# Kernel optimization log

Measured on AMD Instinct MI355X. Metric: run time of the kernel, lower is better.

## Reference

```python
import jax, jax.numpy as jnp
import numpy as np

# Dims: N=batch graphs, V=grid nodes (128x128), D=feature dim, E=edges, L=gnn layers
N, V, D, E, L = 16, 16384, 128, 65536, 2
EPS = 1e-5  # BatchNorm1d default eps


def setup_inputs() -> dict:
    key = jax.random.key(0)
    ks = jax.random.split(key, 8)
    H = jax.random.normal(ks[0], (N, V, D), dtype=jnp.float32)
    edge_src = jax.random.randint(ks[1], (E,), 0, V, dtype=jnp.int32)
    edge_dst = jax.random.randint(ks[2], (E,), 0, V, dtype=jnp.int32)
    A_vals = jax.random.uniform(ks[3], (E,), dtype=jnp.float32)
    scale = 1.0 / np.sqrt(D).astype(np.float32)
    # Stacked per-layer params. Linear stores weight as [out, in]; y = x @ W.T
    W_self = jax.random.normal(ks[4], (L, D, D), dtype=jnp.float32) * scale
    W_nei = jax.random.normal(ks[5], (L, D, D), dtype=jnp.float32) * scale
    gamma = jnp.ones((L, D), dtype=jnp.float32)
    beta = jnp.zeros((L, D), dtype=jnp.float32)
    return {"H": H, "edge_src": edge_src, "edge_dst": edge_dst, "A_vals": A_vals,
            "W_self": W_self, "W_nei": W_nei, "gamma": gamma, "beta": beta}


def reference(H, edge_src, edge_dst, A_vals, W_self, W_nei, gamma, beta):
    X = H  # [N, V, D]
    for l in range(L):
        # SpMM: X_nei[n] = A_norm @ X[n], batched over N via vmap.
        msg = X[:, edge_src, :] * A_vals[None, :, None]  # [N, E, D]
        X_nei = jax.vmap(
            lambda m: jax.ops.segment_sum(m, edge_dst, num_segments=V)
        )(msg)  # [N, V, D]
        # y = x @ W.T for torch Linear(weight=[out,in])
        Y = (jnp.einsum('nvd,ed->nve', X, W_self[l])
             + jnp.einsum('nvd,ed->nve', X_nei, W_nei[l]))  # [N, V, D]
        # BatchNorm1d in training mode over the flattened (N*V) batch dim
        mean = jnp.mean(Y, axis=(0, 1))            # [D]
        var = jnp.var(Y, axis=(0, 1))              # biased variance, [D]
        Y = (Y - mean) * jax.lax.rsqrt(var + EPS) * gamma[l] + beta[l]
        X = jax.nn.relu(Y)
    return X
```

## Files before the change

### kernel.cpp

```cpp
#include <hip/hip_runtime.h>

#define N_ 16
#define V_ 16384
#define D_ 128
#define E_ 65536
#define L_ 2
#define M_ (N_*V_)

typedef __attribute__((ext_vector_type(8))) short short8;
typedef __attribute__((ext_vector_type(4))) float floatx4;

__device__ inline unsigned short f2bf(float x){
  unsigned u = __builtin_bit_cast(unsigned, x);
  unsigned r = u + 0x7fffu + ((u >> 16) & 1u);
  return (unsigned short)(r >> 16);
}
__device__ inline float bf2f(unsigned short h){
  unsigned u = ((unsigned)h) << 16;
  return __builtin_bit_cast(float, u);
}
__device__ inline unsigned pack2(float a, float b){
  return (unsigned)f2bf(a) | ((unsigned)f2bf(b) << 16);
}

__global__ __launch_bounds__(256) void conv_in_k(const float* __restrict__ H,
                                                 unsigned short* __restrict__ Xb){
  int i = blockIdx.x * 256 + threadIdx.x;
  const float4* h4 = (const float4*)H;
  float4 a = h4[2*i], b = h4[2*i+1];
  uint4 o;
  o.x = pack2(a.x, a.y);
  o.y = pack2(a.z, a.w);
  o.z = pack2(b.x, b.y);
  o.w = pack2(b.z, b.w);
  ((uint4*)Xb)[i] = o;
}

__global__ __launch_bounds__(256) void conv_w_k(const float* __restrict__ Wself,
                                                const float* __restrict__ Wnei,
                                                unsigned short* __restrict__ Wb){
  int f = blockIdx.x * 256 + threadIdx.x;
  int lane = f & 63;
  int ct   = (f >> 6) & 7;
  int ks   = (f >> 9) & 3;
  int mat  = (f >> 11) & 1;
  int l    = (f >> 12) & 1;
  int e = ct * 16 + (lane & 15);
  int d = ks * 32 + (lane >> 4) * 8;
  const float* src = (mat ? Wnei : Wself) + ((size_t)l * D_ * D_ + e * D_ + d);
  uint4 o;
  o.x = pack2(src[0], src[1]);
  o.y = pack2(src[2], src[3]);
  o.z = pack2(src[4], src[5]);
  o.w = pack2(src[6], src[7]);
  ((uint4*)Wb)[f] = o;
}

__global__ __launch_bounds__(256) void hist_k(const int* __restrict__ dst, int* __restrict__ cnt){
  int e = blockIdx.x * 256 + threadIdx.x;
  atomicAdd(&cnt[dst[e]], 1);
}

__global__ __launch_bounds__(256) void scan_k(const int* __restrict__ cnt, int* __restrict__ row_ptr){
  __shared__ int part[256];
  int t = threadIdx.x;
  int base = t * 64;
  int s = 0;
  for (int i = 0; i < 64; ++i) s += cnt[base + i];
  part[t] = s;
  __syncthreads();
  for (int d = 1; d < 256; d <<= 1){
    int v = (t >= d) ? part[t - d] : 0;
    __syncthreads();
    part[t] += v;
    __syncthreads();
  }
  int off = part[t] - s;
  for (int i = 0; i < 64; ++i){
    row_ptr[base + i] = off;
    off += cnt[base + i];
  }
  if (t == 255) row_ptr[V_] = off;
}

__global__ __launch_bounds__(256) void scatter_k(const int* __restrict__ src,
                                                 const int* __restrict__ dst,
                                                 const float* __restrict__ vals,
                                                 const int* __restrict__ row_ptr,
                                                 int* __restrict__ fill,
                                                 int* __restrict__ csr_col,
                                                 float* __restrict__ csr_val){
  int e = blockIdx.x * 256 + threadIdx.x;
  int d = dst[e];
  int pos = row_ptr[d] + atomicAdd(&fill[d], 1);
  csr_col[pos] = src[e];
  csr_val[pos] = vals[e];
}

__global__ __launch_bounds__(256) void spmm_k(const unsigned* __restrict__ Xb,
                                              const int* __restrict__ row_ptr,
                                              const int* __restrict__ csr_col,
                                              const float* __restrict__ csr_val,
                                              unsigned* __restrict__ Xnei){
  int v = blockIdx.x;
  int wave = threadIdx.x >> 6;
  int lane = threadIdx.x & 63;
  int r0 = row_ptr[v], r1 = row_ptr[v + 1];
  float acc[4][2] = {};
  for (int i = r0; i < r1; ++i){
    int c = csr_col[i];
    float a = csr_val[i];
#pragma unroll
    for (int t = 0; t < 4; ++t){
      int n = wave + 4 * t;
      unsigned w = Xb[((size_t)n * V_ + c) * 64 + lane];
      acc[t][0] += a * bf2f((unsigned short)(w & 0xffff));
      acc[t][1] += a * bf2f((unsigned short)(w >> 16));
    }
  }
#pragma unroll
  for (int t = 0; t < 4; ++t){
    int n = wave + 4 * t;
    Xnei[((size_t)n * V_ + v) * 64 + lane] = pack2(acc[t][0], acc[t][1]);
  }
}

__global__ __launch_bounds__(256) void gemm_k(const unsigned short* __restrict__ Xb,
                                              const unsigned short* __restrict__ Xnei,
                                              const uint4* __restrict__ Wfrag,
                                              float* __restrict__ Y,
                                              float* __restrict__ stats){
  __shared__ uint4 lds_w[4096];
  int tid = threadIdx.x;
  for (int i = tid; i < 4096; i += 256) lds_w[i] = Wfrag[i];
  __syncthreads();

  int wave = tid >> 6, lane = tid & 63;
  int quad = lane >> 4, l15 = lane & 15;
  int row0 = blockIdx.x * 128 + wave * 32;

  floatx4 zero = {0.f, 0.f, 0.f, 0.f};
  floatx4 acc[2][8];
#pragma unroll
  for (int rt = 0; rt < 2; ++rt)
#pragma unroll
    for (int ct = 0; ct < 8; ++ct) acc[rt][ct] = zero;

  const short8* lw = (const short8*)lds_w;
#pragma unroll
  for (int ks = 0; ks < 4; ++ks){
    short8 a_s[2], a_n[2];
#pragma unroll
    for (int rt = 0; rt < 2; ++rt){
      size_t r = (size_t)(row0 + rt * 16 + l15);
      a_s[rt] = *(const short8*)(Xb   + r * 128 + ks * 32 + quad * 8);
      a_n[rt] = *(const short8*)(Xnei + r * 128 + ks * 32 + quad * 8);
    }
#pragma unroll
    for (int ct = 0; ct < 8; ++ct){
      short8 bs = lw[((0 * 4 + ks) * 8 + ct) * 64 + lane];
      short8 bn = lw[((1 * 4 + ks) * 8 + ct) * 64 + lane];
#pragma unroll
      for (int rt = 0; rt < 2; ++rt){
        acc[rt][ct] = __builtin_amdgcn_mfma_f32_16x16x32_bf16(a_s[rt], bs, acc[rt][ct], 0, 0, 0);
        acc[rt][ct] = __builtin_amdgcn_mfma_f32_16x16x32_bf16(a_n[rt], bn, acc[rt][ct], 0, 0, 0);
      }
    }
  }

  float* sum_base = stats;
  float* sq_base  = stats + 64 * 128;
  int slot = blockIdx.x & 63;
#pragma unroll
  for (int rt = 0; rt < 2; ++rt){
    int rowq = row0 + rt * 16 + quad * 4;
#pragma unroll
    for (int ct = 0; ct < 8; ++ct){
      int col = ct * 16 + l15;
      float s = 0.f, q = 0.f;
#pragma unroll
      for (int rg = 0; rg < 4; ++rg){
        float yv = acc[rt][ct][rg];
        Y[(size_t)(rowq + rg) * 128 + col] = yv;
        s += yv; q += yv * yv;
      }
      s += __shfl_xor(s, 16); s += __shfl_xor(s, 32);
      q += __shfl_xor(q, 16); q += __shfl_xor(q, 32);
      if (lane < 16)      atomicAdd(&sum_base[slot * 128 + ct * 16 + lane], s);
      else if (lane < 32) atomicAdd(&sq_base [slot * 128 + ct * 16 + (lane & 15)], q);
    }
  }
}

__global__ __launch_bounds__(128) void finalize_k(const float* __restrict__ stats,
                                                  const float* __restrict__ gamma,
                                                  const float* __restrict__ beta,
                                                  float* __restrict__ scsh){
  int d = threadIdx.x;
  float s = 0.f, q = 0.f;
  for (int k = 0; k < 64; ++k){
    s += stats[k * 128 + d];
    q += stats[64 * 128 + k * 128 + d];
  }
  float inv = 1.0f / (float)M_;
  float mean = s * inv;
  float var  = q * inv - mean * mean;
  float rstd = rsqrtf(var + 1e-5f);
  float scale = gamma[d] * rstd;
  scsh[d]       = scale;
  scsh[128 + d] = beta[d] - mean * scale;
}

template<int OUT_BF16>
__global__ __launch_bounds__(256) void bn_relu_k(const float* __restrict__ Y,
                                                 const float* __restrict__ scsh,
                                                 float* __restrict__ outf,
                                                 unsigned* __restrict__ outb){
  int i = blockIdx.x * 256 + threadIdx.x;
  int c = (i * 4) & 127;
  float4 y  = ((const float4*)Y)[i];
  float4 sc = *(const float4*)(scsh + c);
  float4 sh = *(const float4*)(scsh + 128 + c);
  float o0 = fmaxf(0.f, y.x * sc.x + sh.x);
  float o1 = fmaxf(0.f, y.y * sc.y + sh.y);
  float o2 = fmaxf(0.f, y.z * sc.z + sh.z);
  float o3 = fmaxf(0.f, y.w * sc.w + sh.w);
  if (OUT_BF16){
    uint2 o; o.x = pack2(o0, o1); o.y = pack2(o2, o3);
    ((uint2*)outb)[i] = o;
  } else {
    float4 o; o.x = o0; o.y = o1; o.z = o2; o.w = o3;
    ((float4*)outf)[i] = o;
  }
}

static inline size_t align_up(size_t x, size_t a){ return (x + a - 1) & ~(a - 1); }

extern "C" void kernel_launch(void* const* d_in, const int* in_sizes, int n_in,
                              void* d_out, int out_size, void* d_ws, size_t ws_size,
                              hipStream_t stream){
  const float* H     = (const float*)d_in[0];
  const int*   esrc  = (const int*)  d_in[1];
  const int*   edst  = (const int*)  d_in[2];
  const float* avals = (const float*)d_in[3];
  const float* Wself = (const float*)d_in[4];
  const float* Wnei  = (const float*)d_in[5];
  const float* gamma = (const float*)d_in[6];
  const float* beta  = (const float*)d_in[7];
  float* Y = (float*)d_out;

  char* ws = (char*)d_ws;
  size_t off = 0;
  unsigned short* Xb   = (unsigned short*)(ws + off); off += align_up((size_t)M_ * D_ * 2, 256);
  unsigned short* Xnei = (unsigned short*)(ws + off); off += align_up((size_t)M_ * D_ * 2, 256);
  unsigned short* Wb   = (unsigned short*)(ws + off); off += align_up((size_t)L_ * 2 * D_ * D_ * 2, 256);
  int*   row_ptr = (int*)  (ws + off); off += align_up((size_t)(V_ + 1) * 4, 256);
  int*   cnt     = (int*)  (ws + off); off += align_up((size_t)V_ * 4, 256);
  int*   csr_col = (int*)  (ws + off); off += align_up((size_t)E_ * 4, 256);
  float* csr_val = (float*)(ws + off); off += align_up((size_t)E_ * 4, 256);
  float* stats   = (float*)(ws + off); off += align_up((size_t)64 * 128 * 2 * 4, 256);
  float* scsh    = (float*)(ws + off); off += align_up((size_t)2 * 128 * 4, 256);
  (void)ws_size; (void)in_sizes; (void)n_in; (void)out_size;

  conv_in_k<<<M_ * D_ / 8 / 256, 256, 0, stream>>>(H, Xb);
  conv_w_k<<<8192 / 256, 256, 0, stream>>>(Wself, Wnei, Wb);

  hipMemsetAsync(cnt, 0, (size_t)V_ * 4, stream);
  hist_k<<<E_ / 256, 256, 0, stream>>>(edst, cnt);
  scan_k<<<1, 256, 0, stream>>>(cnt, row_ptr);
  hipMemsetAsync(cnt, 0, (size_t)V_ * 4, stream);
  scatter_k<<<E_ / 256, 256, 0, stream>>>(esrc, edst, avals, row_ptr, cnt, csr_col, csr_val);

  for (int l = 0; l < L_; ++l){
    spmm_k<<<V_, 256, 0, stream>>>((const unsigned*)Xb, row_ptr, csr_col, csr_val,
                                   (unsigned*)Xnei);
    hipMemsetAsync(stats, 0, (size_t)64 * 128 * 2 * 4, stream);
    gemm_k<<<M_ / 128, 256, 0, stream>>>(Xb, Xnei, (const uint4*)Wb + (size_t)l * 4096,
                                         Y, stats);
    finalize_k<<<1, 128, 0, stream>>>(stats, gamma + l * 128, beta + l * 128, scsh);
    if (l == 0)
      bn_relu_k<1><<<M_ * D_ / 4 / 256, 256, 0, stream>>>(Y, scsh, nullptr, (unsigned*)Xb);
    else
      bn_relu_k<0><<<M_ * D_ / 4 / 256, 256, 0, stream>>>(Y, scsh, Y, nullptr);
  }
}
```

Baseline: 545.4 us.

## Fuse layer-0 BatchNorm+ReLU into next SpMM/GEMM loads and store Y as bf16

Removes the intermediate bn_relu pass between layers by applying the previous layer's scale/shift and ReLU on the fly when SpMM and GEMM load their inputs. The pre-activation Y is now stored as bf16 instead of fp32, and a final kernel expands it to fp32 output. The SpMM is also rearranged so each lane handles four features with 8-byte loads, and the memsets are merged into one. This cuts global memory traffic and launch count, at the price of repeating the normalization per gathered edge and an extra bf16 rounding of Y before BN.

```diff
diff --git a/kernel.cpp b/kernel.cpp
--- a/kernel.cpp
+++ b/kernel.cpp
@@ -97,42 +97,67 @@
   csr_val[pos] = vals[e];
 }
 
-__global__ __launch_bounds__(256) void spmm_k(const unsigned* __restrict__ Xb,
+template<int NORM>
+__global__ __launch_bounds__(256) void spmm_k(const unsigned* __restrict__ X,
                                               const int* __restrict__ row_ptr,
                                               const int* __restrict__ csr_col,
                                               const float* __restrict__ csr_val,
+                                              const float* __restrict__ scsh,
                                               unsigned* __restrict__ Xnei){
   int v = blockIdx.x;
-  int wave = threadIdx.x >> 6;
-  int lane = threadIdx.x & 63;
+  int tid = threadIdx.x;
+  int wave = tid >> 6, lane = tid & 63;
+  int l31 = lane & 31, nh = lane >> 5;
+  float4 sc = {0.f,0.f,0.f,0.f}, sh = {0.f,0.f,0.f,0.f};
+  if (NORM){
+    sc = ((const float4*)scsh)[l31];
+    sh = ((const float4*)(scsh + 128))[l31];
+  }
   int r0 = row_ptr[v], r1 = row_ptr[v + 1];
-  float acc[4][2] = {};
+  float acc[2][4] = {{0.f,0.f,0.f,0.f},{0.f,0.f,0.f,0.f}};
   for (int i = r0; i < r1; ++i){
     int c = csr_col[i];
     float a = csr_val[i];
 #pragma unroll
-    for (int t = 0; t < 4; ++t){
-      int n = wave + 4 * t;
-      unsigned w = Xb[((size_t)n * V_ + c) * 64 + lane];
-      acc[t][0] += a * bf2f((unsigned short)(w & 0xffff));
-      acc[t][1] += a * bf2f((unsigned short)(w >> 16));
-    }
-  }
-#pragma unroll
-  for (int t = 0; t < 4; ++t){
-    int n = wave + 4 * t;
-    Xnei[((size_t)n * V_ + v) * 64 + lane] = pack2(acc[t][0], acc[t][1]);
-  }
-}
-
-__global__ __launch_bounds__(256) void gemm_k(const unsigned short* __restrict__ Xb,
-                                              const unsigned short* __restrict__ Xnei,
-                                              const uint4* __restrict__ Wfrag,
-                                              float* __restrict__ Y,
-                                              float* __restrict__ stats){
+    for (int p = 0; p < 2; ++p){
+      int n = p * 8 + wave * 2 + nh;
+      uint2 w = *((const uint2*)(X + ((size_t)n * V_ + c) * 64) + l31);
+      float x0 = bf2f((unsigned short)(w.x & 0xffff));
+      float x1 = bf2f((unsigned short)(w.x >> 16));
+      float x2 = bf2f((unsigned short)(w.y & 0xffff));
+      float x3 = bf2f((unsigned short)(w.y >> 16));
+      if (NORM){
+        x0 = fmaxf(0.f, x0 * sc.x + sh.x);
+        x1 = fmaxf(0.f, x1 * sc.y + sh.y);
+        x2 = fmaxf(0.f, x2 * sc.z + sh.z);
+        x3 = fmaxf(0.f, x3 * sc.w + sh.w);
+      }
+      acc[p][0] += a * x0; acc[p][1] += a * x1;
+      acc[p][2] += a * x2; acc[p][3] += a * x3;
+    }
+  }
+#pragma unroll
+  for (int p = 0; p < 2; ++p){
+    int n = p * 8 + wave * 2 + nh;
+    uint2 o;
+    o.x = pack2(acc[p][0], acc[p][1]);
+    o.y = pack2(acc[p][2], acc[p][3]);
+    *((uint2*)(Xnei + ((size_t)n * V_ + v) * 64) + l31) = o;
+  }
+}
+
+template<int NORM>
+__global__ __launch_bounds__(256, 2) void gemm_k(const unsigned short* __restrict__ Xs,
+                                                 const unsigned short* __restrict__ Xn,
+                                                 const uint4* __restrict__ Wfrag,
+                                                 const float* __restrict__ scsh,
+                                                 unsigned short* __restrict__ Yb,
+                                                 float* __restrict__ stats){
   __shared__ uint4 lds_w[4096];
+  __shared__ float lds_s[256];
   int tid = threadIdx.x;
   for (int i = tid; i < 4096; i += 256) lds_w[i] = Wfrag[i];
+  if (NORM) lds_s[tid] = scsh[tid];
   __syncthreads();
 
   int wave = tid >> 6, lane = tid & 63;
@@ -149,12 +174,33 @@
   const short8* lw = (const short8*)lds_w;
 #pragma unroll
   for (int ks = 0; ks < 4; ++ks){
+    float scv[8], shv[8];
+    if (NORM){
+      int cb = ks * 32 + quad * 8;
+#pragma unroll
+      for (int j = 0; j < 8; ++j){
+        scv[j] = lds_s[cb + j];
+        shv[j] = lds_s[128 + cb + j];
+      }
+    }
     short8 a_s[2], a_n[2];
 #pragma unroll
     for (int rt = 0; rt < 2; ++rt){
       size_t r = (size_t)(row0 + rt * 16 + l15);
-      a_s[rt] = *(const short8*)(Xb   + r * 128 + ks * 32 + quad * 8);
-      a_n[rt] = *(const short8*)(Xnei + r * 128 + ks * 32 + quad * 8);
+      short8 raw = *(const short8*)(Xs + r * 128 + ks * 32 + quad * 8);
+      if (NORM){
+        short8 t;
+#pragma unroll
+        for (int j = 0; j < 8; ++j){
+          float x = bf2f((unsigned short)raw[j]);
+          x = fmaxf(0.f, x * scv[j] + shv[j]);
+          t[j] = (short)f2bf(x);
+        }
+        a_s[rt] = t;
+      } else {
+        a_s[rt] = raw;
+      }
+      a_n[rt] = *(const short8*)(Xn + r * 128 + ks * 32 + quad * 8);
     }
 #pragma unroll
     for (int ct = 0; ct < 8; ++ct){
@@ -181,7 +227,7 @@
 #pragma unroll
       for (int rg = 0; rg < 4; ++rg){
         float yv = acc[rt][ct][rg];
-        Y[(size_t)(rowq + rg) * 128 + col] = yv;
+        Yb[(size_t)(rowq + rg) * 128 + col] = f2bf(yv);
         s += yv; q += yv * yv;
       }
       s += __shfl_xor(s, 16); s += __shfl_xor(s, 32);
@@ -211,27 +257,27 @@
   scsh[128 + d] = beta[d] - mean * scale;
 }
 
-template<int OUT_BF16>
-__global__ __launch_bounds__(256) void bn_relu_k(const float* __restrict__ Y,
-                                                 const float* __restrict__ scsh,
-                                                 float* __restrict__ outf,
-                                                 unsigned* __restrict__ outb){
+__global__ __launch_bounds__(256) void bn_out_k(const uint4* __restrict__ Y,
+                                                const float* __restrict__ scsh,
+                                                float4* __restrict__ out){
   int i = blockIdx.x * 256 + threadIdx.x;
-  int c = (i * 4) & 127;
-  float4 y  = ((const float4*)Y)[i];
-  float4 sc = *(const float4*)(scsh + c);
-  float4 sh = *(const float4*)(scsh + 128 + c);
-  float o0 = fmaxf(0.f, y.x * sc.x + sh.x);
-  float o1 = fmaxf(0.f, y.y * sc.y + sh.y);
-  float o2 = fmaxf(0.f, y.z * sc.z + sh.z);
-  float o3 = fmaxf(0.f, y.w * sc.w + sh.w);
-  if (OUT_BF16){
-    uint2 o; o.x = pack2(o0, o1); o.y = pack2(o2, o3);
-    ((uint2*)outb)[i] = o;
-  } else {
-    float4 o; o.x = o0; o.y = o1; o.z = o2; o.w = o3;
-    ((float4*)outf)[i] = o;
-  }
+  int c = (i * 8) & 127;
+  uint4 y = Y[i];
+  float4 sc0 = *(const float4*)(scsh + c);
+  float4 sc1 = *(const float4*)(scsh + c + 4);
+  float4 sh0 = *(const float4*)(scsh + 128 + c);
+  float4 sh1 = *(const float4*)(scsh + 132 + c);
+  float4 o0, o1;
+  o0.x = fmaxf(0.f, bf2f((unsigned short)(y.x & 0xffff)) * sc0.x + sh0.x);
+  o0.y = fmaxf(0.f, bf2f((unsigned short)(y.x >> 16))    * sc0.y + sh0.y);
+  o0.z = fmaxf(0.f, bf2f((unsigned short)(y.y & 0xffff)) * sc0.z + sh0.z);
+  o0.w = fmaxf(0.f, bf2f((unsigned short)(y.y >> 16))    * sc0.w + sh0.w);
+  o1.x = fmaxf(0.f, bf2f((unsigned short)(y.z & 0xffff)) * sc1.x + sh1.x);
+  o1.y = fmaxf(0.f, bf2f((unsigned short)(y.z >> 16))    * sc1.y + sh1.y);
+  o1.z = fmaxf(0.f, bf2f((unsigned short)(y.w & 0xffff)) * sc1.z + sh1.z);
+  o1.w = fmaxf(0.f, bf2f((unsigned short)(y.w >> 16))    * sc1.w + sh1.w);
+  out[2 * i]     = o0;
+  out[2 * i + 1] = o1;
 }
 
 static inline size_t align_up(size_t x, size_t a){ return (x + a - 1) & ~(a - 1); }
@@ -247,40 +293,42 @@
   const float* Wnei  = (const float*)d_in[5];
   const float* gamma = (const float*)d_in[6];
   const float* beta  = (const float*)d_in[7];
-  float* Y = (float*)d_out;
 
   char* ws = (char*)d_ws;
   size_t off = 0;
   unsigned short* Xb   = (unsigned short*)(ws + off); off += align_up((size_t)M_ * D_ * 2, 256);
   unsigned short* Xnei = (unsigned short*)(ws + off); off += align_up((size_t)M_ * D_ * 2, 256);
+  unsigned short* Y0   = (unsigned short*)(ws + off); off += align_up((size_t)M_ * D_ * 2, 256);
   unsigned short* Wb   = (unsigned short*)(ws + off); off += align_up((size_t)L_ * 2 * D_ * D_ * 2, 256);
   int*   row_ptr = (int*)  (ws + off); off += align_up((size_t)(V_ + 1) * 4, 256);
-  int*   cnt     = (int*)  (ws + off); off += align_up((size_t)V_ * 4, 256);
   int*   csr_col = (int*)  (ws + off); off += align_up((size_t)E_ * 4, 256);
   float* csr_val = (float*)(ws + off); off += align_up((size_t)E_ * 4, 256);
-  float* stats   = (float*)(ws + off); off += align_up((size_t)64 * 128 * 2 * 4, 256);
-  float* scsh    = (float*)(ws + off); off += align_up((size_t)2 * 128 * 4, 256);
+  float* scsh0   = (float*)(ws + off); off += align_up((size_t)2 * 128 * 4, 256);
+  float* scsh1   = (float*)(ws + off); off += align_up((size_t)2 * 128 * 4, 256);
+  char* zbase = ws + off;
+  int*   cnt    = (int*)  (ws + off); off += (size_t)V_ * 4;
+  int*   fill   = (int*)  (ws + off); off += (size_t)V_ * 4;
+  float* stats0 = (float*)(ws + off); off += (size_t)64 * 128 * 2 * 4;
+  float* stats1 = (float*)(ws + off); off += (size_t)64 * 128 * 2 * 4;
+  size_t zbytes = (size_t)(ws + off - zbase);
+  unsigned short* Y1 = Xb;
   (void)ws_size; (void)in_sizes; (void)n_in; (void)out_size;
 
   conv_in_k<<<M_ * D_ / 8 / 256, 256, 0, stream>>>(H, Xb);
   conv_w_k<<<8192 / 256, 256, 0, stream>>>(Wself, Wnei, Wb);
-
-  hipMemsetAsync(cnt, 0, (size_t)V_ * 4, stream);
+  hipMemsetAsync(zbase, 0, zbytes, stream);
   hist_k<<<E_ / 256, 256, 0, stream>>>(edst, cnt);
   scan_k<<<1, 256, 0, stream>>>(cnt, row_ptr);
-  hipMemsetAsync(cnt, 0, (size_t)V_ * 4, stream);
-  scatter_k<<<E_ / 256, 256, 0, stream>>>(esrc, edst, avals, row_ptr, cnt, csr_col, csr_val);
-
-  for (int l = 0; l < L_; ++l){
-    spmm_k<<<V_, 256, 0, stream>>>((const unsigned*)Xb, row_ptr, csr_col, csr_val,
-                                   (unsigned*)Xnei);
-    hipMemsetAsync(stats, 0, (size_t)64 * 128 * 2 * 4, stream);
-    gemm_k<<<M_ / 128, 256, 0, stream>>>(Xb, Xnei, (const uint4*)Wb + (size_t)l * 4096,
-                                         Y, stats);
-    finalize_k<<<1, 128, 0, stream>>>(stats, gamma + l * 128, beta + l * 128, scsh);
-    if (l == 0)
-      bn_relu_k<1><<<M_ * D_ / 4 / 256, 256, 0, stream>>>(Y, scsh, nullptr, (unsigned*)Xb);
-    else
-      bn_relu_k<0><<<M_ * D_ / 4 / 256, 256, 0, stream>>>(Y, scsh, Y, nullptr);
-  }
-}
+  scatter_k<<<E_ / 256, 256, 0, stream>>>(esrc, edst, avals, row_ptr, fill, csr_col, csr_val);
+
+  spmm_k<0><<<V_, 256, 0, stream>>>((const unsigned*)Xb, row_ptr, csr_col, csr_val,
+                                    nullptr, (unsigned*)Xnei);
+  gemm_k<0><<<M_ / 128, 256, 0, stream>>>(Xb, Xnei, (const uint4*)Wb, nullptr, Y0, stats0);
+  finalize_k<<<1, 128, 0, stream>>>(stats0, gamma, beta, scsh0);
+
+  spmm_k<1><<<V_, 256, 0, stream>>>((const unsigned*)Y0, row_ptr, csr_col, csr_val,
+                                    scsh0, (unsigned*)Xnei);
+  gemm_k<1><<<M_ / 128, 256, 0, stream>>>(Y0, Xnei, (const uint4*)Wb + 4096, scsh0, Y1, stats1);
+  finalize_k<<<1, 128, 0, stream>>>(stats1, gamma + 128, beta + 128, scsh1);
+  bn_out_k<<<M_ * D_ / 8 / 256, 256, 0, stream>>>((const uint4*)Y1, scsh1, (float4*)d_out);
+}
```

Result: faster. 495.5 us (-9.2%).
